# Optimization experiments

Hardware: AMD Instinct MI355X
Metric: run time of the kernel (lower is better)

The kernel has to match this reference:

```python
import jax, jax.numpy as jnp
import numpy as np

K_SIZE, STRIDE, PAD = 3, 2, 1

def _conv1x1(x, w, b):
    return jnp.einsum('bchw,oc->bohw', x, w) + b[None, :, None, None]

def _unfold(x, k, s, p):
    # Matches torch F.unfold ordering: channel-major, then (kh, kw). -> [B, C, k*k, L]
    B, C, H, W = x.shape
    xp = jnp.pad(x, ((0, 0), (0, 0), (p, p), (p, p)))
    ho = (H + 2 * p - k) // s + 1
    wo = (W + 2 * p - k) // s + 1
    cols = []
    for i in range(k):
        for j in range(k):
            cols.append(xp[:, :, i:i + s * (ho - 1) + 1:s, j:j + s * (wo - 1) + 1:s])
    patches = jnp.stack(cols, axis=2)            # [B, C, k*k, ho, wo]
    return patches.reshape(B, C, k * k, ho * wo)

def _forward(shallow, deep, K_w, K_b, KSA_w, KSA_b):
    B, C, H, W = shallow.shape
    d = (2 * C) // 16
    h, w = H // STRIDE, W // STRIDE
    hw = h * w
    max_out = _conv1x1(deep, KSA_w, KSA_b)            # [B, d, h, w]
    # global re-score branch
    max_out1 = jnp.max(max_out, axis=1)               # [B, h, w]
    q = max_out1.reshape(B, hw)                       # [B, hw]
    kt = max_out.reshape(B, hw, d)                    # faithful to torch .view(B,-1,d) (channel-scrambled flat view)
    lit = jnp.einsum('bp,bpd->bd', q, kt) / hw        # mean over hw of outer products -> [B, d]
    V = max_out.reshape(B, d, hw)
    re_score = jnp.einsum('bd,bdp->bp', lit, V).reshape(B, 1, h, w)
    sig = jax.nn.sigmoid(re_score)
    # local windowed attention branch
    Kx = _conv1x1(shallow, K_w, K_b)                  # [B, out, H, W]
    Kunf = _unfold(Kx, K_SIZE, STRIDE, PAD)           # [B, out, kk, hw]
    # torch does matmul([d,1],[1,kk]) then mean over d == mean_d(q_d) * K patch element
    qmean = jnp.mean(max_out, axis=1).reshape(B, 1, 1, hw)
    logits = qmean * Kunf                             # [B, out, kk, hw]
    new_kernel = jax.nn.softmax(logits, axis=2)       # softmax over window dim kk
    att = jnp.sum(new_kernel * Kunf, axis=2)          # [B, out, hw]
    att = att.reshape(B, -1, h, w)
    return sig * att + att, re_score

def setup_inputs():
    key = jax.random.key(0)
    ks = jax.random.split(key, 6)
    B, C, H, W = 4, 256, 128, 128
    out_c, d = 256, (2 * C) // 16
    return {
        'shallow': jax.random.normal(ks[0], (B, C, H, W), jnp.float32),
        'deep': jax.random.normal(ks[1], (B, 2 * C, H // 2, W // 2), jnp.float32),
        'K_w': jax.random.normal(ks[2], (out_c, C), jnp.float32) * 0.02,
        'K_b': jax.random.normal(ks[3], (out_c,), jnp.float32) * 0.02,
        'KSA_w': jax.random.normal(ks[4], (d, 2 * C), jnp.float32) * 0.02,
        'KSA_b': jax.random.normal(ks[5], (d,), jnp.float32) * 0.02,
    }

def reference(shallow, deep, K_w, K_b, KSA_w, KSA_b):
    return _forward(shallow, deep, K_w, K_b, KSA_w, KSA_b)
```

## Files before the change

### kernel.cpp

```cpp
#include <hip/hip_runtime.h>

typedef unsigned short u16;
typedef __attribute__((ext_vector_type(8))) short short8;
typedef __attribute__((ext_vector_type(4))) float float4v;

__device__ __forceinline__ u16 f2bf(float f) {
    unsigned u = __float_as_uint(f);
    u += 0x7FFFu + ((u >> 16) & 1u);
    return (u16)(u >> 16);
}
__device__ __forceinline__ float bf2f(u16 u) {
    return __uint_as_float(((unsigned)u) << 16);
}

__device__ float g_maxout[4 * 32 * 4096];
__device__ float g_q[16384];
__device__ float g_qmean[16384];
__device__ float g_lit[128];
__device__ float g_sigfac[16384];
__device__ u16   g_Kw_bf[65536];
__device__ u16   g_KSAw_bf[16384];
__device__ u16   g_Kx[4 * 256 * 16384];

__global__ __launch_bounds__(256) void prep_kernel(
    const float* __restrict__ Kw, const float* __restrict__ KSAw)
{
    const int idx = blockIdx.x * 256 + threadIdx.x;
    if (idx < 128) g_lit[idx] = 0.f;
    if (idx < 65536) g_Kw_bf[idx] = f2bf(Kw[idx]);
    if (idx < 16384) g_KSAw_bf[idx] = f2bf(KSAw[idx]);
}

__global__ __launch_bounds__(256) void gemm_deep(
    const float* __restrict__ Bias, const float* __restrict__ X)
{
    __shared__ u16 As[16384];
    const int t = threadIdx.x;
    const int wave = t >> 6, lane = t & 63;
    const int quad = lane >> 4, n16 = lane & 15;
    const int b = blockIdx.y;
    const int p = blockIdx.x * 64 + wave * 16 + n16;
    const float* Xb = X + ((long long)b << 21) + p;

#pragma unroll
    for (int c = 0; c < 8; c++) {
        const int idx = (c << 8) + t;
        *(short8*)(As + idx * 8) = *(const short8*)(g_KSAw_bf + idx * 8);
    }

    float breg[2][8];
#pragma unroll
    for (int j = 0; j < 8; j++) breg[0][j] = Xb[((quad << 3) + j) << 12];
#pragma unroll
    for (int j = 0; j < 8; j++) breg[1][j] = Xb[(32 + (quad << 3) + j) << 12];

    __syncthreads();

    float4v acc[2];
#pragma unroll
    for (int i = 0; i < 2; i++) acc[i] = (float4v){0.f, 0.f, 0.f, 0.f};

#pragma unroll
    for (int kb = 0; kb < 16; kb++) {
        const int cur = kb & 1;
        short8 bfrag;
#pragma unroll
        for (int j = 0; j < 8; j++) bfrag[j] = (short)f2bf(breg[cur][j]);
        if (kb < 14) {
            const float* xp = Xb + (((kb + 2) << 5) << 12);
#pragma unroll
            for (int j = 0; j < 8; j++) breg[cur][j] = xp[((quad << 3) + j) << 12];
        }
        const u16* ap = As + n16 * 512 + kb * 32 + quad * 8;
#pragma unroll
        for (int ot = 0; ot < 2; ot++) {
            const short8 afrag = *(const short8*)(ap + ot * 8192);
            acc[ot] = __builtin_amdgcn_mfma_f32_16x16x32_bf16(afrag, bfrag, acc[ot], 0, 0, 0);
        }
    }

    float mx = -3.4e38f, sm = 0.f;
#pragma unroll
    for (int ot = 0; ot < 2; ot++) {
#pragma unroll
        for (int r = 0; r < 4; r++) {
            const int o = ot * 16 + quad * 4 + r;
            const float v = acc[ot][r] + Bias[o];
            g_maxout[((b * 32 + o) << 12) + p] = v;
            mx = fmaxf(mx, v);
            sm += v;
        }
    }
    mx = fmaxf(mx, __shfl_xor(mx, 16, 64));
    sm += __shfl_xor(sm, 16, 64);
    mx = fmaxf(mx, __shfl_xor(mx, 32, 64));
    sm += __shfl_xor(sm, 32, 64);
    if (quad == 0) {
        g_q[(b << 12) + p] = mx;
        g_qmean[(b << 12) + p] = sm * (1.f / 32.f);
    }
}

__global__ __launch_bounds__(256) void lit_kernel()
{
    const int b = blockIdx.y;
    const int f0 = blockIdx.x * 8192;
    const int t = threadIdx.x;
    const float* mo = g_maxout + (b << 17);
    const float* qb = g_q + (b << 12);
    float acc = 0.f;
#pragma unroll
    for (int it = 0; it < 32; it++) {
        const int f = f0 + it * 256 + t;
        acc += qb[f >> 5] * mo[f];
    }
    __shared__ float red[256];
    red[t] = acc;
    __syncthreads();
    if (t < 32) {
        float s = 0.f;
#pragma unroll
        for (int k = 0; k < 8; k++) s += red[t + k * 32];
        atomicAdd(&g_lit[b * 32 + t], s * (1.f / 4096.f));
    }
}

__global__ __launch_bounds__(256) void rescore_kernel(float* __restrict__ out_re)
{
    const int idx = blockIdx.x * 256 + threadIdx.x;
    const int b = idx >> 12, p = idx & 4095;
    const float* mo = g_maxout + (b << 17) + p;
    const float* lb = g_lit + b * 32;
    float r = 0.f;
#pragma unroll
    for (int j = 0; j < 32; j++) r += lb[j] * mo[j << 12];
    out_re[idx] = r;
    g_sigfac[idx] = 1.f + 1.f / (1.f + __expf(-r));
}

__global__ __launch_bounds__(256) void gemm_kx(
    const float* __restrict__ Bias, const float* __restrict__ X)
{
    __shared__ u16 As[2][8192];
    const int t = threadIdx.x;
    const int wave = t >> 6, lane = t & 63;
    const int quad = lane >> 4, n16 = lane & 15;
    const int b = blockIdx.y;
    const int p = blockIdx.x * 64 + wave * 16 + n16;
    const float* Xb = X + ((long long)b << 22) + p;

    const int arow = wave * 64 + (lane >> 2);
    const u16* ag = g_Kw_bf + arow * 256 + (lane & 3) * 8;
    const int alw = wave * 2048 + lane * 8;

    float breg[2][8];
    float4v acc[16];
#pragma unroll
    for (int i = 0; i < 16; i++) acc[i] = (float4v){0.f, 0.f, 0.f, 0.f};

#pragma unroll
    for (int j = 0; j < 8; j++) breg[0][j] = Xb[((quad << 3) + j) << 14];
#pragma unroll
    for (int j = 0; j < 8; j++) breg[1][j] = Xb[(32 + (quad << 3) + j) << 14];
    {
        short8 areg[4];
#pragma unroll
        for (int s = 0; s < 4; s++) areg[s] = *(const short8*)(ag + s * 4096);
#pragma unroll
        for (int s = 0; s < 4; s++) *(short8*)(&As[0][alw + s * 512]) = areg[s];
    }
    __syncthreads();

#pragma unroll
    for (int kb = 0; kb < 8; kb++) {
        const int cur = kb & 1;
        short8 bfrag;
#pragma unroll
        for (int j = 0; j < 8; j++) bfrag[j] = (short)f2bf(breg[cur][j]);

        short8 areg[4];
        if (kb < 6) {
            const float* xp = Xb + (((kb + 2) << 5) << 14);
#pragma unroll
            for (int j = 0; j < 8; j++) breg[cur][j] = xp[((quad << 3) + j) << 14];
        }
        if (kb < 7) {
#pragma unroll
            for (int s = 0; s < 4; s++)
                areg[s] = *(const short8*)(ag + (kb + 1) * 32 + s * 4096);
        }

        const u16* ap = &As[cur][n16 * 32 + quad * 8];
#pragma unroll
        for (int ot = 0; ot < 16; ot++) {
            const short8 afrag = *(const short8*)(ap + ot * 512);
            acc[ot] = __builtin_amdgcn_mfma_f32_16x16x32_bf16(afrag, bfrag, acc[ot], 0, 0, 0);
        }

        if (kb < 7) {
#pragma unroll
            for (int s = 0; s < 4; s++)
                *(short8*)(&As[cur ^ 1][alw + s * 512]) = areg[s];
        }
        __syncthreads();
    }

    u16* kxb = g_Kx + (((long long)b << 8) << 14);
#pragma unroll
    for (int ot = 0; ot < 16; ot++) {
#pragma unroll
        for (int r = 0; r < 4; r++) {
            const int o = ot * 16 + quad * 4 + r;
            kxb[(o << 14) + p] = f2bf(acc[ot][r] + Bias[o]);
        }
    }
}

__global__ __launch_bounds__(256) void att_window(float* __restrict__ out)
{
    __shared__ float tile[9][132];
    const int t = threadIdx.x;
    const int o = blockIdx.y, b = blockIdx.z;
    const int ph0 = blockIdx.x << 2;
    const int y0 = (ph0 << 1) - 1;
    const u16* kxp = g_Kx + ((((long long)b << 8) + o) << 14);

    if (t < 18) tile[t >> 1][(t & 1) ? 129 : 0] = 0.f;
#pragma unroll
    for (int k = 0; k < 5; k++) {
        const int e = (k << 8) + t;
        if (e < 1152) {
            const int r = e >> 7, x = e & 127;
            const int y = y0 + r;
            tile[r][x + 1] = (y >= 0 && y < 128) ? bf2f(kxp[(y << 7) + x]) : 0.f;
        }
    }
    __syncthreads();

    const int p = (blockIdx.x << 8) + t;
    const int pw = t & 63;
    const int rloc = (t >> 6) << 1;
    const float m = g_qmean[(b << 12) + p];
    const float sf = g_sigfac[(b << 12) + p];

    float v[9];
#pragma unroll
    for (int ki = 0; ki < 3; ++ki)
#pragma unroll
        for (int kj = 0; kj < 3; ++kj)
            v[ki * 3 + kj] = tile[rloc + ki][(pw << 1) + kj];

    float mx = -3.4e38f;
#pragma unroll
    for (int k = 0; k < 9; ++k) mx = fmaxf(mx, m * v[k]);
    float s = 0.f, a = 0.f;
#pragma unroll
    for (int k = 0; k < 9; ++k) {
        const float e = __expf(m * v[k] - mx);
        s += e;
        a += e * v[k];
    }
    out[((((long long)b << 8) + o) << 12) + p] = (a / s) * sf;
}

extern "C" void kernel_launch(void* const* d_in, const int* in_sizes, int n_in,
                              void* d_out, int out_size, void* d_ws, size_t ws_size,
                              hipStream_t stream) {
    const float *shallow = 0, *deep = 0, *K_w = 0, *K_b = 0, *KSA_w = 0, *KSA_b = 0;
    for (int i = 0; i < n_in; ++i) {
        switch (in_sizes[i]) {
            case 16777216: shallow = (const float*)d_in[i]; break;
            case 8388608:  deep    = (const float*)d_in[i]; break;
            case 65536:    K_w     = (const float*)d_in[i]; break;
            case 256:      K_b     = (const float*)d_in[i]; break;
            case 16384:    KSA_w   = (const float*)d_in[i]; break;
            case 32:       KSA_b   = (const float*)d_in[i]; break;
        }
    }
    float* out = (float*)d_out;

    prep_kernel<<<320, 256, 0, stream>>>(K_w, KSA_w);
    gemm_deep<<<dim3(64, 4), 256, 0, stream>>>(KSA_b, deep);
    lit_kernel<<<dim3(16, 4), 256, 0, stream>>>();
    rescore_kernel<<<64, 256, 0, stream>>>(out + 4194304);
    gemm_kx<<<dim3(256, 4), 256, 0, stream>>>(K_b, shallow);
    att_window<<<dim3(16, 256, 4), 256, 0, stream>>>(out);
}
```

Before: 183.3 us.

## Restructure Kx GEMM to stage X in swizzled LDS and de-conflict window tile

The 1x1-conv GEMM now holds the weight fragments in registers straight from global memory and stages converted bf16 activation tiles in a 4-deep, XOR-swizzled shared buffer. Each wave computes a 64x64 output block as a 4x4 grid of MFMAs instead of one 16-wide column strip over all 256 outputs. The epilogue writes four contiguous bf16 values per store. The window-attention kernel splits even and odd columns into separate halves of its shared tile so the stride-2 reads avoid bank conflicts. The trade-off is more register pressure from the A fragments and a deeper, more intricate prefetch schedule.

```diff
diff --git a/kernel.cpp b/kernel.cpp
--- a/kernel.cpp
+++ b/kernel.cpp
@@ -3,6 +3,7 @@
 typedef unsigned short u16;
 typedef __attribute__((ext_vector_type(8))) short short8;
 typedef __attribute__((ext_vector_type(4))) float float4v;
+typedef __attribute__((ext_vector_type(4))) unsigned short ushort4v;
 
 __device__ __forceinline__ u16 f2bf(float f) {
     unsigned u = __float_as_uint(f);
@@ -141,114 +142,117 @@
 __global__ __launch_bounds__(256) void gemm_kx(
     const float* __restrict__ Bias, const float* __restrict__ X)
 {
-    __shared__ u16 As[2][8192];
+    __shared__ u16 Bs[4][2048];
     const int t = threadIdx.x;
     const int wave = t >> 6, lane = t & 63;
     const int quad = lane >> 4, n16 = lane & 15;
     const int b = blockIdx.y;
-    const int p = blockIdx.x * 64 + wave * 16 + n16;
-    const float* Xb = X + ((long long)b << 22) + p;
-
-    const int arow = wave * 64 + (lane >> 2);
-    const u16* ag = g_Kw_bf + arow * 256 + (lane & 3) * 8;
-    const int alw = wave * 2048 + lane * 8;
-
+    const int p0 = blockIdx.x * 64;
+    const float* Xb = X + ((long long)b << 22) + p0 + wave * 16 + n16;
+    const u16* Ab = g_Kw_bf + (wave * 64 + n16) * 256 + quad * 8;
+    const int cxor = (n16 >> 1) & 3;
+    const int swz = (quad ^ cxor) << 3;
+    const int bwr = (wave * 16 + n16) * 32 + swz;
+
+    float4v acc[4][4];
+#pragma unroll
+    for (int i = 0; i < 4; i++)
+#pragma unroll
+        for (int j = 0; j < 4; j++) acc[i][j] = (float4v){0.f, 0.f, 0.f, 0.f};
+
+    short8 areg[2][4];
     float breg[2][8];
-    float4v acc[16];
-#pragma unroll
-    for (int i = 0; i < 16; i++) acc[i] = (float4v){0.f, 0.f, 0.f, 0.f};
-
-#pragma unroll
-    for (int j = 0; j < 8; j++) breg[0][j] = Xb[((quad << 3) + j) << 14];
-#pragma unroll
-    for (int j = 0; j < 8; j++) breg[1][j] = Xb[(32 + (quad << 3) + j) << 14];
-    {
-        short8 areg[4];
-#pragma unroll
-        for (int s = 0; s < 4; s++) areg[s] = *(const short8*)(ag + s * 4096);
-#pragma unroll
-        for (int s = 0; s < 4; s++) *(short8*)(&As[0][alw + s * 512]) = areg[s];
-    }
+
+#define BLOAD(dst, kb_) \
+    _Pragma("unroll") for (int j = 0; j < 8; j++) \
+        dst[j] = Xb[(((kb_) << 5) + (quad << 3) + j) << 14];
+#define ALOAD(dst, kb_) \
+    _Pragma("unroll") for (int ot = 0; ot < 4; ot++) \
+        dst[ot] = *(const short8*)(Ab + ot * 4096 + ((kb_) << 5));
+#define BSTORE(src, kb_) { \
+    short8 w_; \
+    _Pragma("unroll") for (int j = 0; j < 8; j++) w_[j] = (short)f2bf(src[j]); \
+    *(short8*)(&Bs[(kb_) & 3][bwr]) = w_; }
+
+    BLOAD(breg[0], 0)
+    BLOAD(breg[1], 1)
+    ALOAD(areg[0], 0)
+    BSTORE(breg[0], 0)
+    BSTORE(breg[1], 1)
+    BLOAD(breg[0], 2)
     __syncthreads();
 
 #pragma unroll
     for (int kb = 0; kb < 8; kb++) {
-        const int cur = kb & 1;
-        short8 bfrag;
-#pragma unroll
-        for (int j = 0; j < 8; j++) bfrag[j] = (short)f2bf(breg[cur][j]);
-
-        short8 areg[4];
-        if (kb < 6) {
-            const float* xp = Xb + (((kb + 2) << 5) << 14);
-#pragma unroll
-            for (int j = 0; j < 8; j++) breg[cur][j] = xp[((quad << 3) + j) << 14];
-        }
-        if (kb < 7) {
-#pragma unroll
-            for (int s = 0; s < 4; s++)
-                areg[s] = *(const short8*)(ag + (kb + 1) * 32 + s * 4096);
-        }
-
-        const u16* ap = &As[cur][n16 * 32 + quad * 8];
-#pragma unroll
-        for (int ot = 0; ot < 16; ot++) {
-            const short8 afrag = *(const short8*)(ap + ot * 512);
-            acc[ot] = __builtin_amdgcn_mfma_f32_16x16x32_bf16(afrag, bfrag, acc[ot], 0, 0, 0);
-        }
-
-        if (kb < 7) {
-#pragma unroll
-            for (int s = 0; s < 4; s++)
-                *(short8*)(&As[cur ^ 1][alw + s * 512]) = areg[s];
-        }
+        const int cr = kb & 1;
+        if (kb < 7) ALOAD(areg[cr ^ 1], kb + 1)
+        if (kb + 3 < 8) BLOAD(breg[cr ^ 1], kb + 3)
+#pragma unroll
+        for (int cg = 0; cg < 4; cg++) {
+            const short8 bfrag = *(const short8*)(&Bs[kb & 3][(cg * 16 + n16) * 32 + swz]);
+#pragma unroll
+            for (int ot = 0; ot < 4; ot++)
+                acc[ot][cg] = __builtin_amdgcn_mfma_f32_16x16x32_bf16(
+                    bfrag, areg[cr][ot], acc[ot][cg], 0, 0, 0);
+        }
+        if (kb + 2 < 8) BSTORE(breg[cr], kb + 2)
         __syncthreads();
     }
+#undef BLOAD
+#undef ALOAD
+#undef BSTORE
 
     u16* kxb = g_Kx + (((long long)b << 8) << 14);
 #pragma unroll
-    for (int ot = 0; ot < 16; ot++) {
-#pragma unroll
-        for (int r = 0; r < 4; r++) {
-            const int o = ot * 16 + quad * 4 + r;
-            kxb[(o << 14) + p] = f2bf(acc[ot][r] + Bias[o]);
+    for (int ot = 0; ot < 4; ot++) {
+        const int o = wave * 64 + ot * 16 + n16;
+        const float bo = Bias[o];
+        u16* orow = kxb + ((long long)o << 14) + p0 + quad * 4;
+#pragma unroll
+        for (int cg = 0; cg < 4; cg++) {
+            ushort4v w;
+#pragma unroll
+            for (int r = 0; r < 4; r++) w[r] = f2bf(acc[ot][cg][r] + bo);
+            *(ushort4v*)(orow + cg * 16) = w;
         }
     }
 }
 
 __global__ __launch_bounds__(256) void att_window(float* __restrict__ out)
 {
-    __shared__ float tile[9][132];
+    __shared__ float tile[9][130];
     const int t = threadIdx.x;
     const int o = blockIdx.y, b = blockIdx.z;
-    const int ph0 = blockIdx.x << 2;
-    const int y0 = (ph0 << 1) - 1;
+    const int y0 = (blockIdx.x << 3) - 1;
     const u16* kxp = g_Kx + ((((long long)b << 8) + o) << 14);
 
-    if (t < 18) tile[t >> 1][(t & 1) ? 129 : 0] = 0.f;
+    if (t < 9) tile[t][64] = 0.f;
 #pragma unroll
     for (int k = 0; k < 5; k++) {
         const int e = (k << 8) + t;
         if (e < 1152) {
             const int r = e >> 7, x = e & 127;
             const int y = y0 + r;
-            tile[r][x + 1] = (y >= 0 && y < 128) ? bf2f(kxp[(y << 7) + x]) : 0.f;
+            const float val = (y >= 0 && y < 128) ? bf2f(kxp[(y << 7) + x]) : 0.f;
+            const int slot = (x & 1) ? (65 + (x >> 1)) : (x >> 1);
+            tile[r][slot] = val;
         }
     }
     __syncthreads();
 
     const int p = (blockIdx.x << 8) + t;
     const int pw = t & 63;
-    const int rloc = (t >> 6) << 1;
+    const int rl = (t >> 6) << 1;
     const float m = g_qmean[(b << 12) + p];
     const float sf = g_sigfac[(b << 12) + p];
 
     float v[9];
 #pragma unroll
-    for (int ki = 0; ki < 3; ++ki)
-#pragma unroll
-        for (int kj = 0; kj < 3; ++kj)
-            v[ki * 3 + kj] = tile[rloc + ki][(pw << 1) + kj];
+    for (int ki = 0; ki < 3; ++ki) {
+        v[ki * 3 + 0] = tile[rl + ki][64 + pw];
+        v[ki * 3 + 1] = tile[rl + ki][pw];
+        v[ki * 3 + 2] = tile[rl + ki][65 + pw];
+    }
 
     float mx = -3.4e38f;
 #pragma unroll
```

Result: slower. 190.3 us (+3.9%).
